# Kernel optimization log

Hardware: AMD Instinct MI355X
Metric: run time of the kernel (lower is better)

Reference implementation:

```python
import math
import jax, jax.numpy as jnp
import numpy as np

E = 1024
H = 16
DH = E // H
R = 8
ALPHA = 16
LORA_S = ALPHA / R

def build_slopes(h):
    start = 2 ** (-2 ** (-(math.log2(h) - 3)))
    return jnp.asarray([start * start ** i for i in range(h)], dtype=jnp.float32)

def setup_inputs() -> dict:
    key = jax.random.key(0)
    ks = jax.random.split(key, 12)
    B, T = 2, 2048
    x = jax.random.normal(ks[0], (B, T, E), dtype=jnp.float32)
    # nn.Linear weights: [out_f, in_f]; LoRA A: [out_f, r], B: [r, in_f]
    def lin(k):
        return jax.random.normal(k, (E, E), dtype=jnp.float32) / math.sqrt(E)
    inp = {
        "x": x,
        "Wq": lin(ks[1]), "Aq": jax.random.normal(ks[2], (E, R)) * 0.01, "Bq": jax.random.normal(ks[3], (R, E)) * 0.01,
        "Wk": lin(ks[4]), "Ak": jax.random.normal(ks[5], (E, R)) * 0.01, "Bk": jax.random.normal(ks[6], (R, E)) * 0.01,
        "Wv": lin(ks[7]), "Av": jax.random.normal(ks[8], (E, R)) * 0.01, "Bv": jax.random.normal(ks[9], (R, E)) * 0.01,
        "Wp": lin(ks[10]),
    }
    return inp

def _lora(x, W, A, Bm):
    # x @ W.T + (x @ B.T) @ A.T * s
    return x @ W.T + ((x @ Bm.T) @ A.T) * LORA_S

def reference(x, Wq, Aq, Bq, Wk, Ak, Bk, Wv, Av, Bv, Wp):
    B, T, _ = x.shape
    slopes = build_slopes(H)  # [H]
    q = _lora(x, Wq, Aq, Bq).reshape(B, T, H, DH).transpose(0, 2, 1, 3)  # [B,H,T,dh]
    k = _lora(x, Wk, Ak, Bk).reshape(B, T, H, DH).transpose(0, 2, 1, 3)
    v = _lora(x, Wv, Av, Bv).reshape(B, T, H, DH).transpose(0, 2, 1, 3)
    s = jnp.einsum("bhqd,bhkd->bhqk", q, k) / math.sqrt(DH)
    i = jnp.arange(T, dtype=jnp.float32)[:, None]
    j = jnp.arange(T, dtype=jnp.float32)[None, :]
    alibi = slopes[:, None, None] * (i - j)  # [H,T,T]
    mask = jnp.triu(jnp.full((T, T), -jnp.inf, dtype=jnp.float32), 1)
    s = s + alibi[None] + mask
    p = jax.nn.softmax(s, axis=-1)
    o = jnp.einsum("bhqk,bhkd->bhqd", p, v).transpose(0, 2, 1, 3).reshape(B, T, E)
    return o @ Wp.T
```

## Files before the change

### kernel.cpp

```cpp
#include <hip/hip_runtime.h>

typedef unsigned short u16;
typedef unsigned int   u32;
typedef __bf16 bf16_t;
typedef bf16_t bf16x8 __attribute__((ext_vector_type(8)));
typedef bf16_t bf16x2v __attribute__((ext_vector_type(2)));
typedef float  f32x4  __attribute__((ext_vector_type(4)));

#define E_DIM 1024
#define T_DIM 2048
#define H_NUM 16
#define DH 64
#define BT 4096
#define Y_LD 2048

__device__ __forceinline__ u16 f2bf(float f) {
  u32 u = __builtin_bit_cast(u32, f);
  u32 r = (u + 0x7fffu + ((u >> 16) & 1u)) >> 16;
  return (u16)r;
}
__device__ __forceinline__ float bf2f(u16 v) {
  u32 u = ((u32)v) << 16;
  return __builtin_bit_cast(float, u);
}

__device__ __forceinline__ float fexp2(float x) {
#if __has_builtin(__builtin_amdgcn_exp2f)
  return __builtin_amdgcn_exp2f(x);
#else
  return exp2f(x);
#endif
}

__device__ __forceinline__ int swz(int r, int c) {
  return r * 64 + (c ^ ((r & 7) << 3));
}

__device__ __forceinline__ void store_val(float* p, float v) { *p = v; }
__device__ __forceinline__ void store_val(u16* p, float v)   { *p = f2bf(v); }

typedef __attribute__((address_space(3))) unsigned int as3_u32;
typedef const __attribute__((address_space(1))) unsigned int as1_u32;

__device__ __forceinline__ void async16(const u16* g, u16* l) {
  __builtin_amdgcn_global_load_lds((as1_u32*)g, (as3_u32*)l, 16, 0, 0);
}

__device__ __forceinline__ void waitvm0_barrier() {
  asm volatile("s_waitcnt vmcnt(0)" ::: "memory");
  __builtin_amdgcn_s_barrier();
  __builtin_amdgcn_sched_barrier(0);
}

__device__ __forceinline__ u32 pack2(float a, float b) {
  bf16x2v v;
  v[0] = (bf16_t)a;
  v[1] = (bf16_t)b;
  return __builtin_bit_cast(u32, v);
}

__device__ __forceinline__ void plswap(u32& a, u32& b) {
#if __has_builtin(__builtin_amdgcn_permlane32_swap)
  typedef u32 u32x2 __attribute__((ext_vector_type(2)));
  u32x2 r = __builtin_amdgcn_permlane32_swap(a, b, false, false);
  a = r[0];
  b = r[1];
#else
  asm volatile("v_permlane32_swap_b32 %0, %1" : "+v"(a), "+v"(b));
#endif
}

__device__ __forceinline__ void redist_pair(u32 A, u32 B, bool odd, u32& wj, u32& wj2) {
  plswap(A, B);
  u32 sA = __builtin_amdgcn_ds_swizzle(A, 0x401F);
  u32 sB = __builtin_amdgcn_ds_swizzle(B, 0x401F);
  wj  = odd ? sB : A;
  wj2 = odd ? B : sA;
}

__global__ __launch_bounds__(256) void k_prep(
    const float* __restrict__ x,
    const float* __restrict__ W0, const float* __restrict__ A0, const float* __restrict__ B0,
    const float* __restrict__ W1, const float* __restrict__ A1, const float* __restrict__ B1,
    const float* __restrict__ W2, const float* __restrict__ A2, const float* __restrict__ B2,
    const float* __restrict__ Wp,
    u16* __restrict__ xb, u16* __restrict__ Weff, u16* __restrict__ Wpb, float s0) {
  const int blk = blockIdx.x;
  const int tid = threadIdx.x;
  if (blk < 4096) {
    int i = (blk * 256 + tid) * 4;
    float4 v = *reinterpret_cast<const float4*>(x + i);
    u32 lo = (u32)f2bf(v.x) | ((u32)f2bf(v.y) << 16);
    u32 hi = (u32)f2bf(v.z) | ((u32)f2bf(v.w) << 16);
    *reinterpret_cast<uint2*>(xb + i) = make_uint2(lo, hi);
  } else if (blk < 7168) {
    int e4 = (blk - 4096) * 256 + tid;
    int m = e4 >> 18;
    int e = (e4 & 262143) * 4;
    const float* W  = (m == 0) ? W0 : (m == 1) ? W1 : W2;
    const float* A  = (m == 0) ? A0 : (m == 1) ? A1 : A2;
    const float* Bm = (m == 0) ? B0 : (m == 1) ? B1 : B2;
    const float sc  = (m == 0) ? s0 : 1.0f;
    int o = e >> 10, i = e & 1023;
    float4 wv = *reinterpret_cast<const float4*>(W + e);
    float acc[4] = {wv.x, wv.y, wv.z, wv.w};
#pragma unroll
    for (int r = 0; r < 8; ++r) {
      float a2 = 2.0f * A[o * 8 + r];
      float4 bv = *reinterpret_cast<const float4*>(Bm + r * 1024 + i);
      acc[0] += a2 * bv.x; acc[1] += a2 * bv.y; acc[2] += a2 * bv.z; acc[3] += a2 * bv.w;
    }
    u32 lo = (u32)f2bf(acc[0] * sc) | ((u32)f2bf(acc[1] * sc) << 16);
    u32 hi = (u32)f2bf(acc[2] * sc) | ((u32)f2bf(acc[3] * sc) << 16);
    *reinterpret_cast<uint2*>(Weff + (size_t)m * 1048576 + e) = make_uint2(lo, hi);
  } else {
    int i = ((blk - 7168) * 256 + tid) * 4;
    float4 v = *reinterpret_cast<const float4*>(Wp + i);
    u32 lo = (u32)f2bf(v.x) | ((u32)f2bf(v.y) << 16);
    u32 hi = (u32)f2bf(v.z) | ((u32)f2bf(v.w) << 16);
    *reinterpret_cast<uint2*>(Wpb + i) = make_uint2(lo, hi);
  }
}

template <typename OUT_T, bool QKV>
__global__ __launch_bounds__(512) void k_gemm2(
    const u16* __restrict__ A, const u16* __restrict__ B,
    OUT_T* __restrict__ C, u16* __restrict__ Vt, int K, int ldc) {
  __shared__ __align__(16) u16 As[2][8192];
  __shared__ __align__(16) u16 Bs[2][8192];
  const int tid  = threadIdx.x;
  const int lane = tid & 63;
  const int wave = tid >> 6;
  const int wr = wave >> 2;
  const int wc = wave & 3;
  const int m0 = blockIdx.y * 128;
  const int n0 = blockIdx.x * 128;
  const int lr = lane & 15;
  const int lk = (lane >> 4) * 8;
  const bool vmode = QKV && (n0 >= 2048);

  f32x4 acc[4][2] = {};

  auto stageg = [&](int bufi, int t) {
    const int k0 = t * 64;
#pragma unroll
    for (int p = 0; p < 2; ++p) {
      const int off = (p * 8 + wave) * 512;
      const int e = off + lane * 8;
      const int r = e >> 6, c = e & 63;
      const int cs = c ^ ((r & 7) << 3);
      async16(&A[(size_t)(m0 + r) * K + t * 64 + cs], &As[bufi][off]);
      async16(&B[(size_t)(n0 + r) * K + t * 64 + cs], &Bs[bufi][off]);
    }
    (void)k0;
  };

  const int nt = K >> 6;
  stageg(0, 0);
  waitvm0_barrier();
  int buf = 0;

  for (int t = 0; t < nt; ++t) {
    if (t + 1 < nt) stageg(buf ^ 1, t + 1);
    __builtin_amdgcn_s_setprio(1);
#pragma unroll
    for (int kk = 0; kk < 2; ++kk) {
      bf16x8 af[4], bfr[2];
#pragma unroll
      for (int mi = 0; mi < 4; ++mi)
        af[mi] = *reinterpret_cast<const bf16x8*>(&As[buf][swz(wr * 64 + mi * 16 + lr, kk * 32 + lk)]);
#pragma unroll
      for (int ni = 0; ni < 2; ++ni)
        bfr[ni] = *reinterpret_cast<const bf16x8*>(&Bs[buf][swz(wc * 32 + ni * 16 + lr, kk * 32 + lk)]);
      if (vmode) {
#pragma unroll
        for (int mi = 0; mi < 4; ++mi)
#pragma unroll
          for (int ni = 0; ni < 2; ++ni)
            acc[mi][ni] = __builtin_amdgcn_mfma_f32_16x16x32_bf16(bfr[ni], af[mi], acc[mi][ni], 0, 0, 0);
      } else {
#pragma unroll
        for (int mi = 0; mi < 4; ++mi)
#pragma unroll
          for (int ni = 0; ni < 2; ++ni)
            acc[mi][ni] = __builtin_amdgcn_mfma_f32_16x16x32_bf16(af[mi], bfr[ni], acc[mi][ni], 0, 0, 0);
      }
    }
    __builtin_amdgcn_s_setprio(0);
    waitvm0_barrier();
    buf ^= 1;
  }

  const int rg = (lane >> 4) * 4;
  if (vmode) {
#pragma unroll
    for (int mi = 0; mi < 4; ++mi)
#pragma unroll
      for (int ni = 0; ni < 2; ++ni)
#pragma unroll
        for (int q = 0; q < 4; ++q) {
          int o = n0 - 2048 + wc * 32 + ni * 16 + rg + q;
          int h = o >> 6, d = o & 63;
          int rowm = m0 + wr * 64 + mi * 16 + lr;
          int b = rowm >> 11, t = rowm & 2047;
          Vt[(size_t)(((b << 4) + h) * 64 + d) * 2048 + t] = f2bf(acc[mi][ni][q]);
        }
  } else {
#pragma unroll
    for (int mi = 0; mi < 4; ++mi)
#pragma unroll
      for (int ni = 0; ni < 2; ++ni)
#pragma unroll
        for (int q = 0; q < 4; ++q) {
          int row = m0 + wr * 64 + mi * 16 + rg + q;
          int col = n0 + wc * 32 + ni * 16 + lr;
          store_val(&C[(size_t)row * ldc + col], acc[mi][ni][q]);
        }
  }
}

__global__ __launch_bounds__(256) void k_attn8(
    const u16* __restrict__ Y, const u16* __restrict__ Vt, u16* __restrict__ Og,
    u16* __restrict__ Oa, u16* __restrict__ Ob,
    float* __restrict__ la, float* __restrict__ lb) {
  __shared__ __align__(16) u16 Ks[2][4096];
  __shared__ __align__(16) u16 Vs[2][4096];

  const int tid = threadIdx.x;
  const int lane = tid & 63;
  const int wave = tid >> 6;
  const int lr = lane & 15;
  const int lg = lane >> 4;
  const int lk = lg * 8;
  const bool odd = (lane & 16) != 0;

  const int orig = blockIdx.x;
  const int bh = orig & 31;
  const int c  = orig >> 5;
  const int qt = (c < 16) ? (16 + c) : (47 - c);
  const int ks = (c >= 16 && c < 32) ? 16 : 0;
  const int ke = (c < 16) ? 15 : qt;
  const int b = bh >> 4, h = bh & 15;

  const float LOG2E = 1.4426950408889634f;
  const float slope2 = exp2f(-0.5f * (float)(h + 1)) * LOG2E;

  const u16* Kb = Y + (size_t)b * T_DIM * Y_LD + 1024 + h * DH;
  const u16* Vb = Vt + (size_t)bh * DH * T_DIM;

  bf16x8 qf[2];
  {
    const int qrow = qt * 64 + wave * 16 + lr;
#pragma unroll
    for (int kk = 0; kk < 2; ++kk)
      qf[kk] = *reinterpret_cast<const bf16x8*>(
          &Y[(size_t)(b * T_DIM + qrow) * Y_LD + h * DH + kk * 32 + lk]);
  }

  float nkb[16];
#pragma unroll
  for (int ni = 0; ni < 4; ++ni)
#pragma unroll
    for (int r = 0; r < 4; ++r)
      nkb[ni * 4 + r] = -slope2 * (float)(ni * 16 + lg * 4 + r) - 12.0f;

  bf16x8 ones;
#pragma unroll
  for (int jj = 0; jj < 8; ++jj) ones[jj] = (bf16_t)1.0f;

  f32x4 oacc[4] = {};
  f32x4 lacc = {};

  auto stage = [&](int bufi, int kt) {
    const int kv0 = kt * 64;
#pragma unroll
    for (int q = 0; q < 2; ++q) {
      const int off = (q * 4 + wave) * 512;
      const int e = off + lane * 8;
      const int r = e >> 6, cc = e & 63;
      const int cs = cc ^ ((r & 7) << 3);
      async16(Kb + (size_t)(kv0 + r) * Y_LD + cs, &Ks[bufi][off]);
      async16(Vb + (size_t)r * T_DIM + kv0 + cs, &Vs[bufi][off]);
    }
  };

  auto step = [&](int kt, int buf, bool DIAG) {
    f32x4 s[4] = {};
    __builtin_amdgcn_s_setprio(1);
#pragma unroll
    for (int kk = 0; kk < 2; ++kk)
#pragma unroll
      for (int ni = 0; ni < 4; ++ni) {
        bf16x8 kf = *reinterpret_cast<const bf16x8*>(&Ks[buf][swz(ni * 16 + lr, kk * 32 + lk)]);
        s[ni] = __builtin_amdgcn_mfma_f32_16x16x32_bf16(kf, qf[kk], s[ni], 0, 0, 0);
      }
    __builtin_amdgcn_s_setprio(0);
    const float ck = -slope2 * (float)(kt * 64);
    u32 pk[4][2];
#pragma unroll
    for (int ni = 0; ni < 4; ++ni) {
      float p[4];
#pragma unroll
      for (int r = 0; r < 4; ++r) {
        float sc = s[ni][r] + nkb[ni * 4 + r] + ck;
        if (DIAG && (ni * 16 + lg * 4 + r) > (wave * 16 + lr)) sc = -INFINITY;
        p[r] = fexp2(sc);
      }
      pk[ni][0] = pack2(p[0], p[1]);
      pk[ni][1] = pack2(p[2], p[3]);
    }
    uint4 PW[2];
#pragma unroll
    for (int kk = 0; kk < 2; ++kk) {
      redist_pair(pk[2 * kk][0], pk[2 * kk + 1][0], odd, PW[kk].x, PW[kk].z);
      redist_pair(pk[2 * kk][1], pk[2 * kk + 1][1], odd, PW[kk].y, PW[kk].w);
    }
    __builtin_amdgcn_s_setprio(1);
#pragma unroll
    for (int kk = 0; kk < 2; ++kk) {
      bf16x8 ph = __builtin_bit_cast(bf16x8, PW[kk]);
      lacc = __builtin_amdgcn_mfma_f32_16x16x32_bf16(ph, ones, lacc, 0, 0, 0);
#pragma unroll
      for (int f = 0; f < 4; ++f) {
        bf16x8 vf = *reinterpret_cast<const bf16x8*>(&Vs[buf][swz(f * 16 + lr, kk * 32 + lk)]);
        oacc[f] = __builtin_amdgcn_mfma_f32_16x16x32_bf16(ph, vf, oacc[f], 0, 0, 0);
      }
    }
    __builtin_amdgcn_s_setprio(0);
  };

  stage(0, ks);
  waitvm0_barrier();
  int buf = 0;
  for (int kt = ks; kt <= ke; ++kt) {
    if (kt < ke) stage(buf ^ 1, kt + 1);
    step(kt, buf, kt == qt);
    waitvm0_barrier();
    buf ^= 1;
  }

  if (c >= 32) {
    float linv[4];
#pragma unroll
    for (int r = 0; r < 4; ++r) linv[r] = 1.0f / lacc[r];
#pragma unroll
    for (int f = 0; f < 4; ++f)
#pragma unroll
      for (int r = 0; r < 4; ++r) {
        int q = qt * 64 + wave * 16 + lg * 4 + r;
        Og[(size_t)(b * T_DIM + q) * E_DIM + h * DH + f * 16 + lr] =
            f2bf(oacc[f][r] * linv[r]);
      }
  } else {
    u16* Op   = (c < 16) ? Oa : Ob;
    float* lp = (c < 16) ? la : lb;
#pragma unroll
    for (int f = 0; f < 4; ++f)
#pragma unroll
      for (int r = 0; r < 4; ++r) {
        int q = qt * 64 + wave * 16 + lg * 4 + r;
        Op[(size_t)(b * 1024 + (q - 1024)) * E_DIM + h * DH + f * 16 + lr] =
            f2bf(oacc[f][r]);
      }
    if (lr == 0) {
#pragma unroll
      for (int r = 0; r < 4; ++r) {
        int q = qt * 64 + wave * 16 + lg * 4 + r;
        lp[bh * 1024 + (q - 1024)] = lacc[r];
      }
    }
  }
}

__global__ __launch_bounds__(256) void k_merge(
    const u16* __restrict__ Oa, const u16* __restrict__ Ob,
    const float* __restrict__ la, const float* __restrict__ lb,
    u16* __restrict__ Og) {
  int idx = blockIdx.x * 256 + threadIdx.x;
  int row = idx >> 8;
  int cg  = (idx & 255) * 4;
  int b = row >> 10, tl = row & 1023;
  int h = cg >> 6;
  size_t po = (size_t)row * E_DIM + cg;
  uint2 ua = *reinterpret_cast<const uint2*>(Oa + po);
  uint2 ub = *reinterpret_cast<const uint2*>(Ob + po);
  float l = la[((b << 4) + h) * 1024 + tl] + lb[((b << 4) + h) * 1024 + tl];
  float inv = 1.0f / l;
  const u16* pa = reinterpret_cast<const u16*>(&ua);
  const u16* pb = reinterpret_cast<const u16*>(&ub);
  u16 o[4];
#pragma unroll
  for (int j = 0; j < 4; ++j)
    o[j] = f2bf((bf2f(pa[j]) + bf2f(pb[j])) * inv);
  *reinterpret_cast<uint2*>(Og + (size_t)(b * T_DIM + 1024 + tl) * E_DIM + cg) =
      *reinterpret_cast<const uint2*>(o);
}

extern "C" void kernel_launch(void* const* d_in, const int* in_sizes, int n_in,
                              void* d_out, int out_size, void* d_ws, size_t ws_size,
                              hipStream_t stream) {
  const float* x  = (const float*)d_in[0];
  const float* Wq = (const float*)d_in[1];
  const float* Aq = (const float*)d_in[2];
  const float* Bq = (const float*)d_in[3];
  const float* Wk = (const float*)d_in[4];
  const float* Ak = (const float*)d_in[5];
  const float* Bk = (const float*)d_in[6];
  const float* Wv = (const float*)d_in[7];
  const float* Av = (const float*)d_in[8];
  const float* Bv = (const float*)d_in[9];
  const float* Wp = (const float*)d_in[10];
  float* out = (float*)d_out;

  char* ws = (char*)d_ws;
  const size_t MB = 1048576;
  u16* xb   = (u16*)(ws);
  u16* Oa   = (u16*)(ws);
  u16* Ob   = (u16*)(ws + 4 * MB);
  u16* Weff = (u16*)(ws + 8 * MB);
  float* la = (float*)(ws + 8 * MB);
  float* lb = (float*)(ws + 8 * MB + 131072);
  u16* Yq   = (u16*)(ws + 14 * MB);
  u16* VtB  = (u16*)(ws + 30 * MB);
  u16* Wpb  = (u16*)(ws + 38 * MB);
  u16* Og   = (u16*)(ws + 40 * MB);

  const float ISQ2 = 0.125f * 1.4426950408889634f;

  k_prep<<<8192, 256, 0, stream>>>(x, Wq, Aq, Bq, Wk, Ak, Bk, Wv, Av, Bv, Wp,
                                   xb, Weff, Wpb, ISQ2);
  {
    dim3 grid(24, 32);
    k_gemm2<u16, true><<<grid, 512, 0, stream>>>(xb, Weff, Yq, VtB, E_DIM, Y_LD);
  }
  k_attn8<<<1536, 256, 0, stream>>>(Yq, VtB, Og, Oa, Ob, la, lb);
  k_merge<<<2048, 256, 0, stream>>>(Oa, Ob, la, lb, Og);
  {
    dim3 grid(8, 32);
    k_gemm2<float, false><<<grid, 512, 0, stream>>>(Og, Wpb, out, nullptr, E_DIM, E_DIM);
  }
}
```

Baseline: 108.7 us.

## Triple-buffer GEMM LDS pipeline, XCD-aware tile mapping, LDS-staged coalesced stores

The QKV and output-projection GEMM moves from double to triple buffering with partial vmcnt waits, so two K-tiles of global loads stay in flight while MFMAs run. Blocks are remapped so that each XCD owns a contiguous set of N column tiles, which should improve L2 reuse of the weight tiles. The bf16 epilogue now stages results through LDS and writes them with 16-byte coalesced stores, including the transposed V output that used to be scattered 2-byte writes. LDS use grows to 96KB, which may limit occupancy.

```diff
diff --git a/kernel.cpp b/kernel.cpp
--- a/kernel.cpp
+++ b/kernel.cpp
@@ -122,19 +122,22 @@
   }
 }
 
-template <typename OUT_T, bool QKV>
-__global__ __launch_bounds__(512) void k_gemm2(
+template <typename OUT_T, bool QKV, int NBX>
+__global__ __launch_bounds__(512) void k_gemm3(
     const u16* __restrict__ A, const u16* __restrict__ B,
     OUT_T* __restrict__ C, u16* __restrict__ Vt, int K, int ldc) {
-  __shared__ __align__(16) u16 As[2][8192];
-  __shared__ __align__(16) u16 Bs[2][8192];
+  __shared__ __align__(16) u16 lds[49152];
   const int tid  = threadIdx.x;
   const int lane = tid & 63;
   const int wave = tid >> 6;
   const int wr = wave >> 2;
   const int wc = wave & 3;
-  const int m0 = blockIdx.y * 128;
-  const int n0 = blockIdx.x * 128;
+  const int oid = blockIdx.x;
+  const int xcd = oid & 7, rest = oid >> 3;
+  const int nb = xcd * NBX + (rest >> 5);
+  const int mb = rest & 31;
+  const int m0 = mb * 128;
+  const int n0 = nb * 128;
   const int lr = lane & 15;
   const int lk = (lane >> 4) * 8;
   const bool vmode = QKV && (n0 >= 2048);
@@ -142,36 +145,39 @@
   f32x4 acc[4][2] = {};
 
   auto stageg = [&](int bufi, int t) {
-    const int k0 = t * 64;
 #pragma unroll
     for (int p = 0; p < 2; ++p) {
       const int off = (p * 8 + wave) * 512;
       const int e = off + lane * 8;
       const int r = e >> 6, c = e & 63;
       const int cs = c ^ ((r & 7) << 3);
-      async16(&A[(size_t)(m0 + r) * K + t * 64 + cs], &As[bufi][off]);
-      async16(&B[(size_t)(n0 + r) * K + t * 64 + cs], &Bs[bufi][off]);
-    }
-    (void)k0;
+      async16(&A[(size_t)(m0 + r) * K + t * 64 + cs], &lds[bufi * 8192 + off]);
+      async16(&B[(size_t)(n0 + r) * K + t * 64 + cs], &lds[24576 + bufi * 8192 + off]);
+    }
   };
 
   const int nt = K >> 6;
   stageg(0, 0);
-  waitvm0_barrier();
-  int buf = 0;
+  stageg(1, 1);
+  asm volatile("s_waitcnt vmcnt(4)" ::: "memory");
+  __builtin_amdgcn_s_barrier();
+  __builtin_amdgcn_sched_barrier(0);
 
   for (int t = 0; t < nt; ++t) {
-    if (t + 1 < nt) stageg(buf ^ 1, t + 1);
+    const int buf = t % 3;
+    if (t + 2 < nt) stageg((t + 2) % 3, t + 2);
     __builtin_amdgcn_s_setprio(1);
 #pragma unroll
     for (int kk = 0; kk < 2; ++kk) {
       bf16x8 af[4], bfr[2];
 #pragma unroll
       for (int mi = 0; mi < 4; ++mi)
-        af[mi] = *reinterpret_cast<const bf16x8*>(&As[buf][swz(wr * 64 + mi * 16 + lr, kk * 32 + lk)]);
+        af[mi] = *reinterpret_cast<const bf16x8*>(
+            &lds[buf * 8192 + swz(wr * 64 + mi * 16 + lr, kk * 32 + lk)]);
 #pragma unroll
       for (int ni = 0; ni < 2; ++ni)
-        bfr[ni] = *reinterpret_cast<const bf16x8*>(&Bs[buf][swz(wc * 32 + ni * 16 + lr, kk * 32 + lk)]);
+        bfr[ni] = *reinterpret_cast<const bf16x8*>(
+            &lds[24576 + buf * 8192 + swz(wc * 32 + ni * 16 + lr, kk * 32 + lk)]);
       if (vmode) {
 #pragma unroll
         for (int mi = 0; mi < 4; ++mi)
@@ -187,24 +193,39 @@
       }
     }
     __builtin_amdgcn_s_setprio(0);
-    waitvm0_barrier();
-    buf ^= 1;
+    if (t + 2 < nt) asm volatile("s_waitcnt vmcnt(4)" ::: "memory");
+    else            asm volatile("s_waitcnt vmcnt(0)" ::: "memory");
+    __builtin_amdgcn_s_barrier();
+    __builtin_amdgcn_sched_barrier(0);
   }
 
   const int rg = (lane >> 4) * 4;
-  if (vmode) {
+  if constexpr (sizeof(OUT_T) == 2) {
 #pragma unroll
     for (int mi = 0; mi < 4; ++mi)
 #pragma unroll
       for (int ni = 0; ni < 2; ++ni)
 #pragma unroll
         for (int q = 0; q < 4; ++q) {
-          int o = n0 - 2048 + wc * 32 + ni * 16 + rg + q;
-          int h = o >> 6, d = o & 63;
-          int rowm = m0 + wr * 64 + mi * 16 + lr;
-          int b = rowm >> 11, t = rowm & 2047;
-          Vt[(size_t)(((b << 4) + h) * 64 + d) * 2048 + t] = f2bf(acc[mi][ni][q]);
+          int rrow, rcol;
+          if (vmode) { rrow = wc * 32 + ni * 16 + rg + q; rcol = wr * 64 + mi * 16 + lr; }
+          else       { rrow = wr * 64 + mi * 16 + rg + q; rcol = wc * 32 + ni * 16 + lr; }
+          lds[rrow * 136 + rcol] = f2bf(acc[mi][ni][q]);
         }
+    __syncthreads();
+    const int r = tid >> 2;
+    const int cs2 = (tid & 3) * 32;
+    const u16* src = &lds[r * 136 + cs2];
+    u16* dst;
+    if (vmode) {
+      int o = n0 - 2048 + r, h = o >> 6, d = o & 63, bb = m0 >> 11;
+      dst = Vt + (size_t)(((bb << 4) + h) * 64 + d) * 2048 + (m0 & 2047) + cs2;
+    } else {
+      dst = (u16*)C + (size_t)(m0 + r) * ldc + n0 + cs2;
+    }
+#pragma unroll
+    for (int j = 0; j < 4; ++j)
+      *reinterpret_cast<uint4*>(dst + j * 8) = *reinterpret_cast<const uint4*>(src + j * 8);
   } else {
 #pragma unroll
     for (int mi = 0; mi < 4; ++mi)
@@ -429,14 +450,8 @@
 
   k_prep<<<8192, 256, 0, stream>>>(x, Wq, Aq, Bq, Wk, Ak, Bk, Wv, Av, Bv, Wp,
                                    xb, Weff, Wpb, ISQ2);
-  {
-    dim3 grid(24, 32);
-    k_gemm2<u16, true><<<grid, 512, 0, stream>>>(xb, Weff, Yq, VtB, E_DIM, Y_LD);
-  }
+  k_gemm3<u16, true, 3><<<768, 512, 0, stream>>>(xb, Weff, Yq, VtB, E_DIM, Y_LD);
   k_attn8<<<1536, 256, 0, stream>>>(Yq, VtB, Og, Oa, Ob, la, lb);
   k_merge<<<2048, 256, 0, stream>>>(Oa, Ob, la, lb, Og);
-  {
-    dim3 grid(8, 32);
-    k_gemm2<float, false><<<grid, 512, 0, stream>>>(Og, Wpb, out, nullptr, E_DIM, E_DIM);
-  }
-}
+  k_gemm3<float, false, 1><<<256, 512, 0, stream>>>(Og, Wpb, out, nullptr, E_DIM, E_DIM);
+}
```

Measured after the change: 118.0 us. 1.09x slower.

## Process two query tiles per attention block to share K/V loads

Applied to the files above, without the earlier changes.

The attention kernel now handles a pair of query tiles per workgroup (one early, one late), so each staged K/V tile feeds two sets of QK and PV MFMAs. This halves the grid and balances causal work per block. The block-to-(batch,head) mapping is also permuted. The cost is more accumulator registers, which may lower occupancy, and fewer blocks in flight.

```diff
diff --git a/kernel.cpp b/kernel.cpp
--- a/kernel.cpp
+++ b/kernel.cpp
@@ -142,7 +142,6 @@
   f32x4 acc[4][2] = {};
 
   auto stageg = [&](int bufi, int t) {
-    const int k0 = t * 64;
 #pragma unroll
     for (int p = 0; p < 2; ++p) {
       const int off = (p * 8 + wave) * 512;
@@ -152,7 +151,6 @@
       async16(&A[(size_t)(m0 + r) * K + t * 64 + cs], &As[bufi][off]);
       async16(&B[(size_t)(n0 + r) * K + t * 64 + cs], &Bs[bufi][off]);
     }
-    (void)k0;
   };
 
   const int nt = K >> 6;
@@ -219,7 +217,7 @@
   }
 }
 
-__global__ __launch_bounds__(256) void k_attn8(
+__global__ __launch_bounds__(256) void k_attn9(
     const u16* __restrict__ Y, const u16* __restrict__ Vt, u16* __restrict__ Og,
     u16* __restrict__ Oa, u16* __restrict__ Ob,
     float* __restrict__ la, float* __restrict__ lb) {
@@ -235,11 +233,12 @@
   const bool odd = (lane & 16) != 0;
 
   const int orig = blockIdx.x;
-  const int bh = orig & 31;
-  const int c  = orig >> 5;
-  const int qt = (c < 16) ? (16 + c) : (47 - c);
-  const int ks = (c >= 16 && c < 32) ? 16 : 0;
-  const int ke = (c < 16) ? 15 : qt;
+  const int bh = (orig & 7) * 4 + ((orig >> 3) & 3);
+  const int g  = orig >> 5;
+  int tq0, tq1, ks, ke;
+  if (g < 8)       { tq0 = 16 + g; tq1 = 31 - g; ks = 0;  ke = 15;  }
+  else if (g < 16) { tq0 = g - 8;  tq1 = 23 - g; ks = 0;  ke = tq1; }
+  else             { tq0 = g;      tq1 = 47 - g; ks = 16; ke = tq1; }
   const int b = bh >> 4, h = bh & 15;
 
   const float LOG2E = 1.4426950408889634f;
@@ -248,12 +247,14 @@
   const u16* Kb = Y + (size_t)b * T_DIM * Y_LD + 1024 + h * DH;
   const u16* Vb = Vt + (size_t)bh * DH * T_DIM;
 
-  bf16x8 qf[2];
-  {
-    const int qrow = qt * 64 + wave * 16 + lr;
+  const int tq[2] = {tq0, tq1};
+  bf16x8 qf[2][2];
+#pragma unroll
+  for (int t = 0; t < 2; ++t) {
+    const int qrow = tq[t] * 64 + wave * 16 + lr;
 #pragma unroll
     for (int kk = 0; kk < 2; ++kk)
-      qf[kk] = *reinterpret_cast<const bf16x8*>(
+      qf[t][kk] = *reinterpret_cast<const bf16x8*>(
           &Y[(size_t)(b * T_DIM + qrow) * Y_LD + h * DH + kk * 32 + lk]);
   }
 
@@ -268,8 +269,8 @@
 #pragma unroll
   for (int jj = 0; jj < 8; ++jj) ones[jj] = (bf16_t)1.0f;
 
-  f32x4 oacc[4] = {};
-  f32x4 lacc = {};
+  f32x4 oacc[2][4] = {};
+  f32x4 lacc[2] = {};
 
   auto stage = [&](int bufi, int kt) {
     const int kv0 = kt * 64;
@@ -284,18 +285,7 @@
     }
   };
 
-  auto step = [&](int kt, int buf, bool DIAG) {
-    f32x4 s[4] = {};
-    __builtin_amdgcn_s_setprio(1);
-#pragma unroll
-    for (int kk = 0; kk < 2; ++kk)
-#pragma unroll
-      for (int ni = 0; ni < 4; ++ni) {
-        bf16x8 kf = *reinterpret_cast<const bf16x8*>(&Ks[buf][swz(ni * 16 + lr, kk * 32 + lk)]);
-        s[ni] = __builtin_amdgcn_mfma_f32_16x16x32_bf16(kf, qf[kk], s[ni], 0, 0, 0);
-      }
-    __builtin_amdgcn_s_setprio(0);
-    const float ck = -slope2 * (float)(kt * 64);
+  auto softmax_pack = [&](const f32x4* s, bool diag, float ck, uint4* PW) {
     u32 pk[4][2];
 #pragma unroll
     for (int ni = 0; ni < 4; ++ni) {
@@ -303,70 +293,96 @@
 #pragma unroll
       for (int r = 0; r < 4; ++r) {
         float sc = s[ni][r] + nkb[ni * 4 + r] + ck;
-        if (DIAG && (ni * 16 + lg * 4 + r) > (wave * 16 + lr)) sc = -INFINITY;
+        if (diag && (ni * 16 + lg * 4 + r) > (wave * 16 + lr)) sc = -INFINITY;
         p[r] = fexp2(sc);
       }
       pk[ni][0] = pack2(p[0], p[1]);
       pk[ni][1] = pack2(p[2], p[3]);
     }
-    uint4 PW[2];
 #pragma unroll
     for (int kk = 0; kk < 2; ++kk) {
       redist_pair(pk[2 * kk][0], pk[2 * kk + 1][0], odd, PW[kk].x, PW[kk].z);
       redist_pair(pk[2 * kk][1], pk[2 * kk + 1][1], odd, PW[kk].y, PW[kk].w);
     }
-    __builtin_amdgcn_s_setprio(1);
-#pragma unroll
-    for (int kk = 0; kk < 2; ++kk) {
-      bf16x8 ph = __builtin_bit_cast(bf16x8, PW[kk]);
-      lacc = __builtin_amdgcn_mfma_f32_16x16x32_bf16(ph, ones, lacc, 0, 0, 0);
-#pragma unroll
-      for (int f = 0; f < 4; ++f) {
-        bf16x8 vf = *reinterpret_cast<const bf16x8*>(&Vs[buf][swz(f * 16 + lr, kk * 32 + lk)]);
-        oacc[f] = __builtin_amdgcn_mfma_f32_16x16x32_bf16(ph, vf, oacc[f], 0, 0, 0);
-      }
-    }
-    __builtin_amdgcn_s_setprio(0);
   };
 
   stage(0, ks);
   waitvm0_barrier();
   int buf = 0;
+
   for (int kt = ks; kt <= ke; ++kt) {
     if (kt < ke) stage(buf ^ 1, kt + 1);
-    step(kt, buf, kt == qt);
+    const bool do0 = (kt <= tq0);
+    f32x4 s1[4] = {}, s0[4] = {};
+    __builtin_amdgcn_s_setprio(1);
+#pragma unroll
+    for (int kk = 0; kk < 2; ++kk)
+#pragma unroll
+      for (int ni = 0; ni < 4; ++ni) {
+        bf16x8 kf = *reinterpret_cast<const bf16x8*>(&Ks[buf][swz(ni * 16 + lr, kk * 32 + lk)]);
+        s1[ni] = __builtin_amdgcn_mfma_f32_16x16x32_bf16(kf, qf[1][kk], s1[ni], 0, 0, 0);
+        if (do0) s0[ni] = __builtin_amdgcn_mfma_f32_16x16x32_bf16(kf, qf[0][kk], s0[ni], 0, 0, 0);
+      }
+    __builtin_amdgcn_s_setprio(0);
+    const float ck = -slope2 * (float)(kt * 64);
+    uint4 PW1[2], PW0[2];
+    softmax_pack(s1, kt == tq1, ck, PW1);
+    if (do0) softmax_pack(s0, kt == tq0, ck, PW0);
+    __builtin_amdgcn_s_setprio(1);
+#pragma unroll
+    for (int kk = 0; kk < 2; ++kk) {
+      bf16x8 ph = __builtin_bit_cast(bf16x8, PW1[kk]);
+      bf16x8 pl = ph;
+      if (do0) pl = __builtin_bit_cast(bf16x8, PW0[kk]);
+      lacc[1] = __builtin_amdgcn_mfma_f32_16x16x32_bf16(ph, ones, lacc[1], 0, 0, 0);
+      if (do0) lacc[0] = __builtin_amdgcn_mfma_f32_16x16x32_bf16(pl, ones, lacc[0], 0, 0, 0);
+#pragma unroll
+      for (int f = 0; f < 4; ++f) {
+        bf16x8 vf = *reinterpret_cast<const bf16x8*>(&Vs[buf][swz(f * 16 + lr, kk * 32 + lk)]);
+        oacc[1][f] = __builtin_amdgcn_mfma_f32_16x16x32_bf16(ph, vf, oacc[1][f], 0, 0, 0);
+        if (do0) oacc[0][f] = __builtin_amdgcn_mfma_f32_16x16x32_bf16(pl, vf, oacc[0][f], 0, 0, 0);
+      }
+    }
+    __builtin_amdgcn_s_setprio(0);
     waitvm0_barrier();
     buf ^= 1;
   }
 
-  if (c >= 32) {
-    float linv[4];
-#pragma unroll
-    for (int r = 0; r < 4; ++r) linv[r] = 1.0f / lacc[r];
-#pragma unroll
-    for (int f = 0; f < 4; ++f)
-#pragma unroll
-      for (int r = 0; r < 4; ++r) {
-        int q = qt * 64 + wave * 16 + lg * 4 + r;
-        Og[(size_t)(b * T_DIM + q) * E_DIM + h * DH + f * 16 + lr] =
-            f2bf(oacc[f][r] * linv[r]);
-      }
+  const bool direct = (ks == 0) && (ke >= tq1);
+  if (direct) {
+#pragma unroll
+    for (int t = 0; t < 2; ++t) {
+      float linv[4];
+#pragma unroll
+      for (int r = 0; r < 4; ++r) linv[r] = 1.0f / lacc[t][r];
+#pragma unroll
+      for (int f = 0; f < 4; ++f)
+#pragma unroll
+        for (int r = 0; r < 4; ++r) {
+          int q = tq[t] * 64 + wave * 16 + lg * 4 + r;
+          Og[(size_t)(b * T_DIM + q) * E_DIM + h * DH + f * 16 + lr] =
+              f2bf(oacc[t][f][r] * linv[r]);
+        }
+    }
   } else {
-    u16* Op   = (c < 16) ? Oa : Ob;
-    float* lp = (c < 16) ? la : lb;
-#pragma unroll
-    for (int f = 0; f < 4; ++f)
-#pragma unroll
-      for (int r = 0; r < 4; ++r) {
-        int q = qt * 64 + wave * 16 + lg * 4 + r;
-        Op[(size_t)(b * 1024 + (q - 1024)) * E_DIM + h * DH + f * 16 + lr] =
-            f2bf(oacc[f][r]);
-      }
-    if (lr == 0) {
-#pragma unroll
-      for (int r = 0; r < 4; ++r) {
-        int q = qt * 64 + wave * 16 + lg * 4 + r;
-        lp[bh * 1024 + (q - 1024)] = lacc[r];
+    u16* Op   = (ks == 0) ? Oa : Ob;
+    float* lp = (ks == 0) ? la : lb;
+#pragma unroll
+    for (int t = 0; t < 2; ++t) {
+#pragma unroll
+      for (int f = 0; f < 4; ++f)
+#pragma unroll
+        for (int r = 0; r < 4; ++r) {
+          int q = tq[t] * 64 + wave * 16 + lg * 4 + r;
+          Op[(size_t)(b * 1024 + (q - 1024)) * E_DIM + h * DH + f * 16 + lr] =
+              f2bf(oacc[t][f][r]);
+        }
+      if (lr == 0) {
+#pragma unroll
+        for (int r = 0; r < 4; ++r) {
+          int q = tq[t] * 64 + wave * 16 + lg * 4 + r;
+          lp[bh * 1024 + (q - 1024)] = lacc[t][r];
+        }
       }
     }
   }
@@ -433,7 +449,7 @@
     dim3 grid(24, 32);
     k_gemm2<u16, true><<<grid, 512, 0, stream>>>(xb, Weff, Yq, VtB, E_DIM, Y_LD);
   }
-  k_attn8<<<1536, 256, 0, stream>>>(Yq, VtB, Og, Oa, Ob, la, lb);
+  k_attn9<<<768, 256, 0, stream>>>(Yq, VtB, Og, Oa, Ob, la, lb);
   k_merge<<<2048, 256, 0, stream>>>(Oa, Ob, la, lb, Og);
   {
     dim3 grid(8, 32);
```

Measured after the change: 129.5 us. 19.1% more time.
